# Kernel optimization log

Measured on AMD Instinct MI355X. Metric: run time of the kernel, lower is better.

The kernel has to match this reference:

```python
import jax, jax.numpy as jnp
import numpy as np

HEADS = 16
HIDDEN = 1024
D_HEAD = HIDDEN // HEADS
SCALE = float(D_HEAD) ** 0.5


def setup_inputs() -> dict:
    key = jax.random.key(0)
    ks = jax.random.split(key, 11)
    B, L = 2, 2048
    x = jax.random.normal(ks[0], (B, L, HIDDEN), dtype=jnp.float32)
    # 0/1 padding mask, broadcast over heads and query positions
    mask = jax.random.randint(ks[1], (B, 1, 1, L), 0, 2).astype(jnp.float32)
    s = 1.0 / np.sqrt(HIDDEN)
    Wq = jax.random.normal(ks[2], (HIDDEN, HIDDEN), dtype=jnp.float32) * s
    bq = jax.random.normal(ks[3], (HIDDEN,), dtype=jnp.float32) * s
    Wk = jax.random.normal(ks[4], (HIDDEN, HIDDEN), dtype=jnp.float32) * s
    bk = jax.random.normal(ks[5], (HIDDEN,), dtype=jnp.float32) * s
    Wv = jax.random.normal(ks[6], (HIDDEN, HIDDEN), dtype=jnp.float32) * s
    bv = jax.random.normal(ks[7], (HIDDEN,), dtype=jnp.float32) * s
    Wo = jax.random.normal(ks[8], (HIDDEN, HIDDEN), dtype=jnp.float32) * s
    bo = jax.random.normal(ks[9], (HIDDEN,), dtype=jnp.float32) * s
    return {"x": x, "mask": mask, "Wq": Wq, "bq": bq, "Wk": Wk, "bk": bk,
            "Wv": Wv, "bv": bv, "Wo": Wo, "bo": bo}


def reference(x, mask, Wq, bq, Wk, bk, Wv, bv, Wo, bo):
    B, L, _ = x.shape
    # projections (Linear: x @ W + b), split heads -> [B, H, L, Dh]
    def proj(W, b):
        return (jnp.dot(x, W) + b).reshape(B, L, HEADS, D_HEAD).transpose(0, 2, 1, 3)
    q = proj(Wq, bq)
    k = proj(Wk, bk)
    v = proj(Wv, bv)
    # scaled dot-product with additive mask: scores [B, H, Lq, Lk]
    scores = jnp.einsum('bhqd,bhkd->bhqk', q, k) / SCALE + mask * (-10000.0)
    attn = jax.nn.softmax(scores, axis=-1)  # dropout p=0.0 -> identity
    out = jnp.einsum('bhqk,bhkd->bhqd', attn, v)
    out = out.transpose(0, 2, 1, 3).reshape(B, L, HIDDEN)
    return jnp.dot(out, Wo) + bo
```

## Files before the change

kernel.cpp:

```cpp
#include <hip/hip_runtime.h>
#include <math.h>

typedef unsigned short u16;
typedef short v8s __attribute__((ext_vector_type(8)));
typedef float v4f __attribute__((ext_vector_type(4)));

#define HIDDEN 1024
#define L_SEQ 2048
#define NH 16
#define DH 64
#define PADS 72
#define NKMAX 1280

#define QSCALE 0.18033688011112042f

__device__ __forceinline__ u16 f2bf(float f) {
  union { float f; unsigned int i; } c; c.f = f;
  unsigned int x = c.i;
  unsigned int r = (x + 0x7fffu + ((x >> 16) & 1u)) >> 16;
  return (u16)r;
}

#if defined(__has_builtin)
#if __has_builtin(__builtin_amdgcn_cvt_pk_bf16_f32)
#define HAS_PKBF 1
#endif
#endif

__device__ __forceinline__ unsigned pkbf(float a, float b) {
#ifdef HAS_PKBF
  typedef __bf16 v2bf __attribute__((ext_vector_type(2)));
  union { v2bf v; unsigned u; } c;
  c.v = __builtin_amdgcn_cvt_pk_bf16_f32(a, b);
  return c.u;
#else
  return (unsigned)f2bf(a) | ((unsigned)f2bf(b) << 16);
#endif
}

__device__ __forceinline__ void gload16(const void* g, void* l) {
  void* gg = const_cast<void*>(g);
  __builtin_amdgcn_global_load_lds(
      (__attribute__((address_space(1))) void*)gg,
      (__attribute__((address_space(3))) void*)l, 16, 0, 0);
}

__global__ __launch_bounds__(256) void prep(
    const float* __restrict__ x, u16* __restrict__ xb,
    const float* __restrict__ Wq, const float* __restrict__ Wk,
    const float* __restrict__ Wv, const float* __restrict__ Wo,
    u16* __restrict__ WtQ, u16* __restrict__ WtK,
    u16* __restrict__ WtV, u16* __restrict__ WtO,
    const float* __restrict__ maskg, u16* __restrict__ keep,
    unsigned* __restrict__ nkslot) {
  const int bid = blockIdx.x;
  const int t = threadIdx.x;

  if (bid < 2048) {
    const int i = (bid * 256 + t) * 8;
    const float4 a = *(const float4*)(x + i);
    const float4 b = *(const float4*)(x + i + 4);
    unsigned o[4] = {pkbf(a.x, a.y), pkbf(a.z, a.w), pkbf(b.x, b.y), pkbf(b.z, b.w)};
    *(uint4*)(xb + i) = *(const uint4*)o;
    return;
  }

  if (bid < 6144) {
    const int m = bid - 2048;
    const int z = m >> 10;
    const int rem = m & 1023;
    const int bx = rem & 31, by = rem >> 5;
    const float* src; u16* dst;
    if (z == 0) { src = Wq; dst = WtQ; }
    else if (z == 1) { src = Wk; dst = WtK; }
    else if (z == 2) { src = Wv; dst = WtV; }
    else { src = Wo; dst = WtO; }

    __shared__ u16 tile[32][33];
    const int tx = t & 31, ty = t >> 5;
    const int xcol = bx * 32 + tx;
    const int y0 = by * 32;
#pragma unroll
    for (int i = ty; i < 32; i += 8)
      tile[i][tx] = f2bf(src[(size_t)(y0 + i) * HIDDEN + xcol]);
    __syncthreads();
    const int xo = y0 + tx;
#pragma unroll
    for (int i = ty; i < 32; i += 8)
      dst[(size_t)(bx * 32 + i) * HIDDEN + xo] = tile[tx][i];
    return;
  }

  if (t < 64) {
    const int b = bid - 6144;
    const int lane = t;
    const float* mp = maskg + b * L_SEQ;
    int cnt = 0;
#pragma unroll 1
    for (int j = 0; j < 32; ++j) cnt += (mp[lane * 32 + j] == 0.0f) ? 1 : 0;
    int inc = cnt;
#pragma unroll
    for (int off = 1; off < 64; off <<= 1) {
      const int v = __shfl_up(inc, off, 64);
      if (lane >= off) inc += v;
    }
    int base = inc - cnt;
    u16* kp = keep + b * L_SEQ;
#pragma unroll 1
    for (int j = 0; j < 32; ++j) {
      const int k = lane * 32 + j;
      if (mp[k] == 0.0f) kp[base++] = (u16)k;
    }
    const int total = __shfl(inc, 63, 64);
    for (int i = total + lane; i < NKMAX; i += 64) kp[i] = 0;
    if (lane == 0) nkslot[b] = (unsigned)total;
  }
}

__global__ __launch_bounds__(256) void gemm128(
    const u16* __restrict__ A,
    const u16* __restrict__ B0, const u16* __restrict__ B1, const u16* __restrict__ B2,
    const float* __restrict__ bias0, const float* __restrict__ bias1, const float* __restrict__ bias2,
    u16* __restrict__ C0, u16* __restrict__ C1, u16* __restrict__ C2,
    float* __restrict__ Cf, const u16* __restrict__ keep,
    const unsigned* __restrict__ nkslot,
    int qkv_mode) {
  __shared__ __align__(16) u16 As[128 * 32];
  __shared__ __align__(16) u16 Bs[128 * 32];

  const u16* Bt; const float* bias; u16* C;
  if (blockIdx.z == 0) { Bt = B0; bias = bias0; C = C0; }
  else if (blockIdx.z == 1) { Bt = B1; bias = bias1; C = C1; }
  else { Bt = B2; bias = bias2; C = C2; }
  const int mode = qkv_mode ? (blockIdx.z == 0 ? 1 : (blockIdx.z == 1 ? 2 : 3)) : 0;
  const float oscale = (mode == 1) ? QSCALE : 1.0f;

  const int t = threadIdx.x;
  const int lane = t & 63;
  const int wave = t >> 6;
  const int quad = lane >> 4;
  const int l16 = lane & 15;
  const int wm = wave >> 1;
  const int wn = wave & 1;

  const int n0 = blockIdx.x * 128;
  const int sr = t >> 2;
  const int sc = (t & 3) * 8;

  int m0 = blockIdx.y * 128;
  int kvb = 0;
  const u16* Ag0;
  const u16* Ag1;
  if (mode == 2 || mode == 3) {
    const int y = blockIdx.y;
    if (y >= 20) return;
    kvb = y / 10;
    m0 = (y % 10) * 128;
    const unsigned nk = nkslot[kvb];
    if ((unsigned)m0 >= ((nk + 63u) & ~63u)) return;
    const int sr0 = keep[kvb * L_SEQ + m0 + sr];
    const int sr1 = keep[kvb * L_SEQ + m0 + 64 + sr];
    Ag0 = A + ((size_t)(kvb * L_SEQ + sr0)) * HIDDEN + sc;
    Ag1 = A + ((size_t)(kvb * L_SEQ + sr1)) * HIDDEN + sc;
  } else {
    Ag0 = A + (size_t)(m0 + sr) * HIDDEN + sc;
    Ag1 = Ag0 + (size_t)64 * HIDDEN;
  }
  const u16* Bg0 = Bt + (size_t)(n0 + sr) * HIDDEN + sc;
  const u16* Bg1 = Bg0 + (size_t)64 * HIDDEN;
  u16* Al0 = &As[sr * 32 + sc];
  u16* Al1 = &As[(64 + sr) * 32 + sc];
  u16* Bl0 = &Bs[sr * 32 + sc];
  u16* Bl1 = &Bs[(64 + sr) * 32 + sc];

  v4f acc[4][4];
#pragma unroll
  for (int mi = 0; mi < 4; ++mi)
#pragma unroll
    for (int ni = 0; ni < 4; ++ni)
      acc[mi][ni] = (v4f){0.f, 0.f, 0.f, 0.f};

  for (int k0 = 0; k0 < HIDDEN; k0 += 32) {
    __syncthreads();
    gload16(Ag0 + k0, Al0);
    gload16(Ag1 + k0, Al1);
    gload16(Bg0 + k0, Bl0);
    gload16(Bg1 + k0, Bl1);
    __syncthreads();

    v8s a[4], b[4];
#pragma unroll
    for (int mi = 0; mi < 4; ++mi)
      a[mi] = *(const v8s*)&As[(wm * 64 + mi * 16 + l16) * 32 + quad * 8];
#pragma unroll
    for (int ni = 0; ni < 4; ++ni)
      b[ni] = *(const v8s*)&Bs[(wn * 64 + ni * 16 + l16) * 32 + quad * 8];
#pragma unroll
    for (int mi = 0; mi < 4; ++mi)
#pragma unroll
      for (int ni = 0; ni < 4; ++ni)
        acc[mi][ni] = __builtin_amdgcn_mfma_f32_16x16x32_bf16(a[mi], b[ni], acc[mi][ni], 0, 0, 0);
  }

#pragma unroll
  for (int ni = 0; ni < 4; ++ni) {
    const int col = n0 + wn * 64 + ni * 16 + l16;
    const float bv = bias[col];
#pragma unroll
    for (int mi = 0; mi < 4; ++mi) {
      const int row0 = m0 + wm * 64 + mi * 16 + quad * 4;
      const float v0 = (acc[mi][ni][0] + bv) * oscale;
      const float v1 = (acc[mi][ni][1] + bv) * oscale;
      const float v2 = (acc[mi][ni][2] + bv) * oscale;
      const float v3 = (acc[mi][ni][3] + bv) * oscale;
      if (mode == 0) {
        Cf[(size_t)(row0 + 0) * HIDDEN + col] = v0;
        Cf[(size_t)(row0 + 1) * HIDDEN + col] = v1;
        Cf[(size_t)(row0 + 2) * HIDDEN + col] = v2;
        Cf[(size_t)(row0 + 3) * HIDDEN + col] = v3;
      } else if (mode == 1) {
        const int hh = col >> 6, d = col & 63;
        const float vv[4] = {v0, v1, v2, v3};
#pragma unroll
        for (int i = 0; i < 4; ++i) {
          const int rr = row0 + i;
          const int bb = rr >> 11, l = rr & 2047;
          C[((size_t)(bb * NH + hh) * L_SEQ + l) * DH + d] = f2bf(vv[i]);
        }
      } else if (mode == 2) {
        const int hh = col >> 6, d = col & 63;
        const float vv[4] = {v0, v1, v2, v3};
#pragma unroll
        for (int i = 0; i < 4; ++i)
          C[((size_t)(kvb * NH + hh) * L_SEQ + row0 + i) * DH + d] = f2bf(vv[i]);
      } else {
        const int hh = col >> 6, d = col & 63;
        unsigned pk[2] = {pkbf(v0, v1), pkbf(v2, v3)};
        *(uint2*)&C[((size_t)((kvb * NH + hh) * DH + d)) * L_SEQ + row0] = *(const uint2*)pk;
      }
    }
  }
}

__global__ __launch_bounds__(256) void attn64(
    const u16* __restrict__ Qg, const u16* __restrict__ Kcg, const u16* __restrict__ VTg,
    const float* __restrict__ maskg, u16* __restrict__ Og) {
  __shared__ __align__(16) u16 Qs[64 * PADS];
  __shared__ __align__(16) u16 Ks[64 * PADS];
  __shared__ __align__(16) u16 Vt[64 * PADS];
  __shared__ int s_nk;
  u16* Ps = Qs;

  const int t = threadIdx.x;
  const int lane = t & 63;
  const int wave = t >> 6;
  const int quad = lane >> 4;
  const int l16 = lane & 15;

  const int q0 = blockIdx.x * 64;
  const int bh = blockIdx.y;
  const int b = bh >> 4;
  const int h = bh & 15;

  const size_t base = (size_t)bh * L_SEQ * DH;
  const u16* Qp = Qg + base;
  const u16* Kp = Kcg + base;
  const u16* VTp = VTg + base;

  if (t == 0) s_nk = 0;
  __syncthreads();
  {
    int cnt = 0;
    const float4* m4 = (const float4*)(maskg + b * L_SEQ);
    for (int e = t; e < 512; e += 256) {
      const float4 mv = m4[e];
      cnt += (mv.x == 0.f) + (mv.y == 0.f) + (mv.z == 0.f) + (mv.w == 0.f);
    }
#pragma unroll
    for (int off = 1; off < 64; off <<= 1) cnt += __shfl_xor(cnt, off, 64);
    if (lane == 0) atomicAdd(&s_nk, cnt);
  }

  const int r = t >> 3, c = (t & 7) * 8;
  *(uint4*)&Qs[r * PADS + c] = *(const uint4*)&Qp[(size_t)(q0 + r) * DH + c];
  *(uint4*)&Qs[(r + 32) * PADS + c] = *(const uint4*)&Qp[(size_t)(q0 + r + 32) * DH + c];
  __syncthreads();

  const int nkb = s_nk;
  const int nkpad = (nkb + 63) & ~63;

  const v8s qf0 = *(const v8s*)&Qs[(wave * 16 + l16) * PADS + quad * 8];
  const v8s qf1 = *(const v8s*)&Qs[(wave * 16 + l16) * PADS + 32 + quad * 8];

  const v8s ones = {0x3F80, 0x3F80, 0x3F80, 0x3F80, 0x3F80, 0x3F80, 0x3F80, 0x3F80};

  v4f o[4], o4 = (v4f){0.f, 0.f, 0.f, 0.f};
#pragma unroll
  for (int ti = 0; ti < 4; ++ti) o[ti] = (v4f){0.f, 0.f, 0.f, 0.f};

  uint4 ka = *(const uint4*)&Kp[(size_t)r * DH + c];
  uint4 kb = *(const uint4*)&Kp[(size_t)(r + 32) * DH + c];
  uint4 va = *(const uint4*)&VTp[(size_t)r * L_SEQ + c];
  uint4 vb = *(const uint4*)&VTp[(size_t)(r + 32) * L_SEQ + c];

  for (int k0 = 0; k0 < nkpad; k0 += 64) {
    __syncthreads();
    *(uint4*)&Ks[r * PADS + c] = ka;
    *(uint4*)&Ks[(r + 32) * PADS + c] = kb;
    if (k0 + 64 <= nkb) {
      *(uint4*)&Vt[r * PADS + c] = va;
      *(uint4*)&Vt[(r + 32) * PADS + c] = vb;
    } else {
      const u16* vsa = (const u16*)&va;
      const u16* vsb = (const u16*)&vb;
#pragma unroll
      for (int j = 0; j < 8; ++j) {
        const bool ok = (k0 + c + j) < nkb;
        Vt[r * PADS + c + j] = ok ? vsa[j] : (u16)0;
        Vt[(r + 32) * PADS + c + j] = ok ? vsb[j] : (u16)0;
      }
    }
    __syncthreads();

    if (k0 + 64 < nkpad) {
      ka = *(const uint4*)&Kp[(size_t)(k0 + 64 + r) * DH + c];
      kb = *(const uint4*)&Kp[(size_t)(k0 + 64 + r + 32) * DH + c];
      va = *(const uint4*)&VTp[(size_t)r * L_SEQ + k0 + 64 + c];
      vb = *(const uint4*)&VTp[(size_t)(r + 32) * L_SEQ + k0 + 64 + c];
    }

#pragma unroll
    for (int ni = 0; ni < 4; ++ni) {
      v4f s = (v4f){0.f, 0.f, 0.f, 0.f};
      const v8s kf0 = *(const v8s*)&Ks[(ni * 16 + l16) * PADS + quad * 8];
      const v8s kf1 = *(const v8s*)&Ks[(ni * 16 + l16) * PADS + 32 + quad * 8];
      s = __builtin_amdgcn_mfma_f32_16x16x32_bf16(qf0, kf0, s, 0, 0, 0);
      s = __builtin_amdgcn_mfma_f32_16x16x32_bf16(qf1, kf1, s, 0, 0, 0);
      float p0, p1, p2, p3;
      if (k0 + 64 <= nkb) {
        p0 = exp2f(s[0]); p1 = exp2f(s[1]); p2 = exp2f(s[2]); p3 = exp2f(s[3]);
      } else {
        const bool inr = (k0 + ni * 16 + l16) < nkb;
        p0 = inr ? exp2f(s[0]) : 0.f;
        p1 = inr ? exp2f(s[1]) : 0.f;
        p2 = inr ? exp2f(s[2]) : 0.f;
        p3 = inr ? exp2f(s[3]) : 0.f;
      }
      const unsigned pa = pkbf(p0, p1), pb = pkbf(p2, p3);
      const int rb = wave * 16 + quad * 4;
      const int cb = ni * 16 + l16;
      Ps[(rb + 0) * PADS + cb] = (u16)(pa & 0xffff);
      Ps[(rb + 1) * PADS + cb] = (u16)(pa >> 16);
      Ps[(rb + 2) * PADS + cb] = (u16)(pb & 0xffff);
      Ps[(rb + 3) * PADS + cb] = (u16)(pb >> 16);
    }

    const v8s pf0 = *(const v8s*)&Ps[(wave * 16 + l16) * PADS + quad * 8];
    const v8s pf1 = *(const v8s*)&Ps[(wave * 16 + l16) * PADS + 32 + quad * 8];

    o4 = __builtin_amdgcn_mfma_f32_16x16x32_bf16(pf0, ones, o4, 0, 0, 0);
    o4 = __builtin_amdgcn_mfma_f32_16x16x32_bf16(pf1, ones, o4, 0, 0, 0);

#pragma unroll
    for (int ti = 0; ti < 4; ++ti) {
      const v8s vf0 = *(const v8s*)&Vt[(ti * 16 + l16) * PADS + quad * 8];
      const v8s vf1 = *(const v8s*)&Vt[(ti * 16 + l16) * PADS + 32 + quad * 8];
      o[ti] = __builtin_amdgcn_mfma_f32_16x16x32_bf16(pf0, vf0, o[ti], 0, 0, 0);
      o[ti] = __builtin_amdgcn_mfma_f32_16x16x32_bf16(pf1, vf1, o[ti], 0, 0, 0);
    }
  }

  float linv[4];
#pragma unroll
  for (int i = 0; i < 4; ++i) linv[i] = 1.0f / o4[i];

#pragma unroll
  for (int ti = 0; ti < 4; ++ti) {
#pragma unroll
    for (int i = 0; i < 4; ++i) {
      const int q = q0 + wave * 16 + quad * 4 + i;
      const int d = ti * 16 + l16;
      Og[(size_t)(b * L_SEQ + q) * HIDDEN + h * DH + d] = f2bf(o[ti][i] * linv[i]);
    }
  }
}

extern "C" void kernel_launch(void* const* d_in, const int* in_sizes, int n_in,
                              void* d_out, int out_size, void* d_ws, size_t ws_size,
                              hipStream_t stream) {
  const float* x    = (const float*)d_in[0];
  const float* mask = (const float*)d_in[1];
  const float* Wq   = (const float*)d_in[2];
  const float* bq   = (const float*)d_in[3];
  const float* Wk   = (const float*)d_in[4];
  const float* bk   = (const float*)d_in[5];
  const float* Wv   = (const float*)d_in[6];
  const float* bv   = (const float*)d_in[7];
  const float* Wo   = (const float*)d_in[8];
  const float* bo   = (const float*)d_in[9];
  float* out = (float*)d_out;
  u16* ws = (u16*)d_ws;

  const unsigned M1 = 1u << 20;
  u16* WtQ = ws;
  u16* WtK = ws + M1;
  u16* WtV = ws + 2 * M1;
  u16* WtO = ws + 3 * M1;
  u16* xb  = ws + 4 * M1;
  u16* Qb  = ws + 8 * M1;
  u16* Kc  = ws + 12 * M1;
  u16* VTc = ws + 16 * M1;
  u16* Ob  = ws + 20 * M1;
  u16* keep = ws + 24 * M1 - 4096;
  unsigned* nkslot = (unsigned*)(ws + 24 * M1 - 4096 - 8);

  prep<<<6146, 256, 0, stream>>>(x, xb, Wq, Wk, Wv, Wo, WtQ, WtK, WtV, WtO,
                                 mask, keep, nkslot);
  gemm128<<<dim3(8, 32, 3), 256, 0, stream>>>(xb, WtQ, WtK, WtV, bq, bk, bv,
                                              Qb, Kc, VTc, nullptr, keep, nkslot, 1);
  attn64<<<dim3(32, 32), 256, 0, stream>>>(Qb, Kc, VTc, mask, Ob);
  gemm128<<<dim3(8, 32, 1), 256, 0, stream>>>(Ob, WtO, WtO, WtO, bo, bo, bo,
                                              nullptr, nullptr, nullptr, out, nullptr, nullptr, 0);
}
```

Before: 199.5 us.

## Double-buffer K/V tiles with direct global-to-LDS loads and XOR-swizzled layout

The attention kernel now streams K and V^T tiles straight into a double-buffered LDS region with gload16, so the next tile loads while the current one is computed, and one barrier per tile is dropped. The padded shared arrays become an XOR-swizzled layout to avoid bank conflicts. The score MFMA operands are swapped so P can be written back as packed 32-bit stores. The per-block mask count is replaced by reading the key count the prep kernel already computed. Partial tiles now need an explicit zero-fill pass over V in LDS, and workspace offsets for keep and nkslot move, which risks aliasing with other buffers.

```diff
diff --git a/kernel.cpp b/kernel.cpp
--- a/kernel.cpp
+++ b/kernel.cpp
@@ -9,7 +9,6 @@
 #define L_SEQ 2048
 #define NH 16
 #define DH 64
-#define PADS 72
 #define NKMAX 1280
 
 #define QSCALE 0.18033688011112042f
@@ -244,18 +243,15 @@
 
 __global__ __launch_bounds__(256) void attn64(
     const u16* __restrict__ Qg, const u16* __restrict__ Kcg, const u16* __restrict__ VTg,
-    const float* __restrict__ maskg, u16* __restrict__ Og) {
-  __shared__ __align__(16) u16 Qs[64 * PADS];
-  __shared__ __align__(16) u16 Ks[64 * PADS];
-  __shared__ __align__(16) u16 Vt[64 * PADS];
-  __shared__ int s_nk;
-  u16* Ps = Qs;
+    const unsigned* __restrict__ nkslot, u16* __restrict__ Og) {
+  __shared__ __align__(16) u16 lds[20480];
 
   const int t = threadIdx.x;
   const int lane = t & 63;
-  const int wave = t >> 6;
+  const int w = t >> 6;
   const int quad = lane >> 4;
   const int l16 = lane & 15;
+  const int e7 = l16 & 7;
 
   const int q0 = blockIdx.x * 64;
   const int bh = blockIdx.y;
@@ -267,30 +263,34 @@
   const u16* Kp = Kcg + base;
   const u16* VTp = VTg + base;
 
-  if (t == 0) s_nk = 0;
+  const int nkb = (int)nkslot[b];
+  const int nkpad = (nkb + 63) & ~63;
+  const int ntiles = nkpad >> 6;
+
+  const int r8 = lane >> 3;
+  const int sl = lane & 7;
+  const int og8 = (sl ^ r8) * 8;
+  const int koff = (w * 16 + r8) * DH + og8;
+  const int voff = (w * 16 + r8) * L_SEQ + og8;
+
+  gload16(Kp + koff, &lds[(w * 16) * 64]);
+  gload16(Kp + koff + 8 * DH, &lds[(w * 16 + 8) * 64]);
+  gload16(VTp + voff, &lds[8192 + (w * 16) * 64]);
+  gload16(VTp + voff + 8 * L_SEQ, &lds[8192 + (w * 16 + 8) * 64]);
+
+  {
+    const int r = t >> 3, oc = t & 7;
+    *(uint4*)&lds[16384 + r * 64 + ((oc ^ (r & 7)) * 8)] =
+        *(const uint4*)&Qp[(size_t)(q0 + r) * DH + oc * 8];
+    const int r2 = r + 32;
+    *(uint4*)&lds[16384 + r2 * 64 + ((oc ^ (r2 & 7)) * 8)] =
+        *(const uint4*)&Qp[(size_t)(q0 + r2) * DH + oc * 8];
+  }
   __syncthreads();
-  {
-    int cnt = 0;
-    const float4* m4 = (const float4*)(maskg + b * L_SEQ);
-    for (int e = t; e < 512; e += 256) {
-      const float4 mv = m4[e];
-      cnt += (mv.x == 0.f) + (mv.y == 0.f) + (mv.z == 0.f) + (mv.w == 0.f);
-    }
-#pragma unroll
-    for (int off = 1; off < 64; off <<= 1) cnt += __shfl_xor(cnt, off, 64);
-    if (lane == 0) atomicAdd(&s_nk, cnt);
-  }
-
-  const int r = t >> 3, c = (t & 7) * 8;
-  *(uint4*)&Qs[r * PADS + c] = *(const uint4*)&Qp[(size_t)(q0 + r) * DH + c];
-  *(uint4*)&Qs[(r + 32) * PADS + c] = *(const uint4*)&Qp[(size_t)(q0 + r + 32) * DH + c];
-  __syncthreads();
-
-  const int nkb = s_nk;
-  const int nkpad = (nkb + 63) & ~63;
-
-  const v8s qf0 = *(const v8s*)&Qs[(wave * 16 + l16) * PADS + quad * 8];
-  const v8s qf1 = *(const v8s*)&Qs[(wave * 16 + l16) * PADS + 32 + quad * 8];
+
+  const int rowq = 16384 + (w * 16 + l16) * 64;
+  const v8s qf0 = *(const v8s*)&lds[rowq + ((quad ^ e7) * 8)];
+  const v8s qf1 = *(const v8s*)&lds[rowq + (((4 + quad) ^ e7) * 8)];
 
   const v8s ones = {0x3F80, 0x3F80, 0x3F80, 0x3F80, 0x3F80, 0x3F80, 0x3F80, 0x3F80};
 
@@ -298,73 +298,64 @@
 #pragma unroll
   for (int ti = 0; ti < 4; ++ti) o[ti] = (v4f){0.f, 0.f, 0.f, 0.f};
 
-  uint4 ka = *(const uint4*)&Kp[(size_t)r * DH + c];
-  uint4 kb = *(const uint4*)&Kp[(size_t)(r + 32) * DH + c];
-  uint4 va = *(const uint4*)&VTp[(size_t)r * L_SEQ + c];
-  uint4 vb = *(const uint4*)&VTp[(size_t)(r + 32) * L_SEQ + c];
-
-  for (int k0 = 0; k0 < nkpad; k0 += 64) {
+  for (int n = 0; n < ntiles; ++n) {
     __syncthreads();
-    *(uint4*)&Ks[r * PADS + c] = ka;
-    *(uint4*)&Ks[(r + 32) * PADS + c] = kb;
-    if (k0 + 64 <= nkb) {
-      *(uint4*)&Vt[r * PADS + c] = va;
-      *(uint4*)&Vt[(r + 32) * PADS + c] = vb;
-    } else {
-      const u16* vsa = (const u16*)&va;
-      const u16* vsb = (const u16*)&vb;
-#pragma unroll
-      for (int j = 0; j < 8; ++j) {
-        const bool ok = (k0 + c + j) < nkb;
-        Vt[r * PADS + c + j] = ok ? vsa[j] : (u16)0;
-        Vt[(r + 32) * PADS + c + j] = ok ? vsb[j] : (u16)0;
+    const int ksb = (n & 1) * 4096;
+    const int vtb = 8192 + (n & 1) * 4096;
+    if (n + 1 < ntiles) {
+      const int k1 = (n + 1) * 64;
+      const int ksb2 = ((n + 1) & 1) * 4096;
+      const int vtb2 = 8192 + ((n + 1) & 1) * 4096;
+      gload16(Kp + (size_t)k1 * DH + koff, &lds[ksb2 + (w * 16) * 64]);
+      gload16(Kp + (size_t)k1 * DH + koff + 8 * DH, &lds[ksb2 + (w * 16 + 8) * 64]);
+      gload16(VTp + voff + k1, &lds[vtb2 + (w * 16) * 64]);
+      gload16(VTp + voff + k1 + 8 * L_SEQ, &lds[vtb2 + (w * 16 + 8) * 64]);
+    }
+    const int k0 = n * 64;
+    const bool partial = (k0 + 64 > nkb);
+    if (partial) {
+      for (int e = t; e < 4096; e += 256) {
+        const int d = e >> 6, cc = e & 63;
+        if (k0 + cc >= nkb)
+          lds[vtb + d * 64 + (((cc >> 3) ^ (d & 7)) * 8) + (cc & 7)] = 0;
       }
-    }
-    __syncthreads();
-
-    if (k0 + 64 < nkpad) {
-      ka = *(const uint4*)&Kp[(size_t)(k0 + 64 + r) * DH + c];
-      kb = *(const uint4*)&Kp[(size_t)(k0 + 64 + r + 32) * DH + c];
-      va = *(const uint4*)&VTp[(size_t)r * L_SEQ + k0 + 64 + c];
-      vb = *(const uint4*)&VTp[(size_t)(r + 32) * L_SEQ + k0 + 64 + c];
+      __syncthreads();
     }
 
 #pragma unroll
     for (int ni = 0; ni < 4; ++ni) {
+      const int rowk = ksb + (ni * 16 + l16) * 64;
+      const v8s kf0 = *(const v8s*)&lds[rowk + ((quad ^ e7) * 8)];
+      const v8s kf1 = *(const v8s*)&lds[rowk + (((4 + quad) ^ e7) * 8)];
       v4f s = (v4f){0.f, 0.f, 0.f, 0.f};
-      const v8s kf0 = *(const v8s*)&Ks[(ni * 16 + l16) * PADS + quad * 8];
-      const v8s kf1 = *(const v8s*)&Ks[(ni * 16 + l16) * PADS + 32 + quad * 8];
-      s = __builtin_amdgcn_mfma_f32_16x16x32_bf16(qf0, kf0, s, 0, 0, 0);
-      s = __builtin_amdgcn_mfma_f32_16x16x32_bf16(qf1, kf1, s, 0, 0, 0);
+      s = __builtin_amdgcn_mfma_f32_16x16x32_bf16(kf0, qf0, s, 0, 0, 0);
+      s = __builtin_amdgcn_mfma_f32_16x16x32_bf16(kf1, qf1, s, 0, 0, 0);
       float p0, p1, p2, p3;
-      if (k0 + 64 <= nkb) {
+      if (!partial) {
         p0 = exp2f(s[0]); p1 = exp2f(s[1]); p2 = exp2f(s[2]); p3 = exp2f(s[3]);
       } else {
-        const bool inr = (k0 + ni * 16 + l16) < nkb;
-        p0 = inr ? exp2f(s[0]) : 0.f;
-        p1 = inr ? exp2f(s[1]) : 0.f;
-        p2 = inr ? exp2f(s[2]) : 0.f;
-        p3 = inr ? exp2f(s[3]) : 0.f;
+        const int kb = k0 + ni * 16 + quad * 4;
+        p0 = (kb + 0 < nkb) ? exp2f(s[0]) : 0.f;
+        p1 = (kb + 1 < nkb) ? exp2f(s[1]) : 0.f;
+        p2 = (kb + 2 < nkb) ? exp2f(s[2]) : 0.f;
+        p3 = (kb + 3 < nkb) ? exp2f(s[3]) : 0.f;
       }
-      const unsigned pa = pkbf(p0, p1), pb = pkbf(p2, p3);
-      const int rb = wave * 16 + quad * 4;
-      const int cb = ni * 16 + l16;
-      Ps[(rb + 0) * PADS + cb] = (u16)(pa & 0xffff);
-      Ps[(rb + 1) * PADS + cb] = (u16)(pa >> 16);
-      Ps[(rb + 2) * PADS + cb] = (u16)(pb & 0xffff);
-      Ps[(rb + 3) * PADS + cb] = (u16)(pb >> 16);
-    }
-
-    const v8s pf0 = *(const v8s*)&Ps[(wave * 16 + l16) * PADS + quad * 8];
-    const v8s pf1 = *(const v8s*)&Ps[(wave * 16 + l16) * PADS + 32 + quad * 8];
+      const int slo = rowq + (((ni * 2 + (quad >> 1)) ^ e7) * 8) + (quad & 1) * 4;
+      *(unsigned*)&lds[slo] = pkbf(p0, p1);
+      *(unsigned*)&lds[slo + 2] = pkbf(p2, p3);
+    }
+
+    const v8s pf0 = *(const v8s*)&lds[rowq + ((quad ^ e7) * 8)];
+    const v8s pf1 = *(const v8s*)&lds[rowq + (((4 + quad) ^ e7) * 8)];
 
     o4 = __builtin_amdgcn_mfma_f32_16x16x32_bf16(pf0, ones, o4, 0, 0, 0);
     o4 = __builtin_amdgcn_mfma_f32_16x16x32_bf16(pf1, ones, o4, 0, 0, 0);
 
 #pragma unroll
     for (int ti = 0; ti < 4; ++ti) {
-      const v8s vf0 = *(const v8s*)&Vt[(ti * 16 + l16) * PADS + quad * 8];
-      const v8s vf1 = *(const v8s*)&Vt[(ti * 16 + l16) * PADS + 32 + quad * 8];
+      const int rowv = vtb + (ti * 16 + l16) * 64;
+      const v8s vf0 = *(const v8s*)&lds[rowv + ((quad ^ e7) * 8)];
+      const v8s vf1 = *(const v8s*)&lds[rowv + (((4 + quad) ^ e7) * 8)];
       o[ti] = __builtin_amdgcn_mfma_f32_16x16x32_bf16(pf0, vf0, o[ti], 0, 0, 0);
       o[ti] = __builtin_amdgcn_mfma_f32_16x16x32_bf16(pf1, vf1, o[ti], 0, 0, 0);
     }
@@ -378,7 +369,7 @@
   for (int ti = 0; ti < 4; ++ti) {
 #pragma unroll
     for (int i = 0; i < 4; ++i) {
-      const int q = q0 + wave * 16 + quad * 4 + i;
+      const int q = q0 + w * 16 + quad * 4 + i;
       const int d = ti * 16 + l16;
       Og[(size_t)(b * L_SEQ + q) * HIDDEN + h * DH + d] = f2bf(o[ti][i] * linv[i]);
     }
@@ -411,14 +402,14 @@
   u16* Kc  = ws + 12 * M1;
   u16* VTc = ws + 16 * M1;
   u16* Ob  = ws + 20 * M1;
-  u16* keep = ws + 24 * M1 - 4096;
-  unsigned* nkslot = (unsigned*)(ws + 24 * M1 - 4096 - 8);
+  u16* keep = ws + 16 * M1 - 8192;
+  unsigned* nkslot = (unsigned*)(ws + 16 * M1 - 8192 - 8);
 
   prep<<<6146, 256, 0, stream>>>(x, xb, Wq, Wk, Wv, Wo, WtQ, WtK, WtV, WtO,
                                  mask, keep, nkslot);
   gemm128<<<dim3(8, 32, 3), 256, 0, stream>>>(xb, WtQ, WtK, WtV, bq, bk, bv,
                                               Qb, Kc, VTc, nullptr, keep, nkslot, 1);
-  attn64<<<dim3(32, 32), 256, 0, stream>>>(Qb, Kc, VTc, mask, Ob);
+  attn64<<<dim3(32, 32), 256, 0, stream>>>(Qb, Kc, VTc, nkslot, Ob);
   gemm128<<<dim3(8, 32, 1), 256, 0, stream>>>(Ob, WtO, WtO, WtO, bo, bo, bo,
                                               nullptr, nullptr, nullptr, out, nullptr, nullptr, 0);
 }
```

New measurement: 199.4 us. Within noise of the previous version (-0.1%).
